# Kernel tuning notes

Measured on AMD Instinct MI355X. Metric: run time of the kernel, lower is better.

## Reference

```python
import jax, jax.numpy as jnp
import numpy as np

N = 250000           # points
B = 2                # batch size
GX, GY, GZ = 256, 256, 32   # voxel grid
SCALES = (2, 4, 6, 8)
CIN = 64             # input_channels
CR = 64              # reduce_channels
CH = CR // 2         # hidden = reduce_channels // 2
COUT = 64            # output_channels


def _cdiv(a, b):
    return -(-a // b)


def setup_inputs() -> dict:
    key = jax.random.key(0)
    ks = jax.random.split(key, 16)
    x = jax.random.normal(ks[0], (N, CIN), jnp.float32)
    bcol = jax.random.randint(ks[1], (N, 1), 0, B)
    xy = jax.random.randint(ks[2], (N, 2), 0, GX)
    z = jax.random.randint(ks[3], (N, 1), 0, GZ)
    coords = jnp.concatenate([bcol, xy, z], axis=1).astype(jnp.int32)
    coords_inv = jnp.arange(N, dtype=jnp.int32)

    def lin(k, fan_in, shape):
        return jax.random.normal(k, shape, jnp.float32) / np.sqrt(fan_in)

    return {
        "x": x,
        "coords": coords,
        "coords_inv": coords_inv,
        "W_red": lin(ks[4], CIN, (CIN, CR)),
        "b_red": jnp.zeros((CR,), jnp.float32),
        "W_pool": lin(ks[5], CR, (len(SCALES), CR, CH)),   # fc_list
        "b_pool": jnp.zeros((len(SCALES), CH), jnp.float32),
        "W_att": lin(ks[6], CH, (len(SCALES), CH, CH)),    # fcs
        "b_att": jnp.zeros((len(SCALES), CH), jnp.float32),
        "W_z": lin(ks[7], CH, (CH, CH)),                   # self.fc (no bias)
        "W_out": lin(ks[8], CH, (CH, CR)),                 # out_fc (no bias)
        "W_l1": lin(ks[9], 2 * CR, (2 * CR, CR)),          # linear_output[0] (no bias)
        "W_l2": lin(ks[10], CR, (CR, COUT)),               # linear_output[2]
        "b_l2": jnp.zeros((COUT,), jnp.float32),
    }


def reference(x, coords, coords_inv, W_red, b_red, W_pool, b_pool,
              W_att, b_att, W_z, W_out, W_l1, W_l2, b_l2):
    # feature_reduce + ReLU
    red = jax.nn.relu(x @ W_red + b_red)              # [N, CR]
    bidx = coords[:, 0].astype(jnp.int32)
    cxyz = coords[:, 1:]

    outs = []
    for j, ps in enumerate(SCALES):
        gx, gy, gz = _cdiv(GX, ps), _cdiv(GY, ps), _cdiv(GZ, ps)
        q = cxyz // ps                                 # quantized coords
        seg = ((bidx * gx + q[:, 0]) * gy + q[:, 1]) * gz + q[:, 2]
        ns = B * gx * gy * gz
        # scatter_mean over voxels at this scale
        sums = jax.ops.segment_sum(red, seg, num_segments=ns)
        cnt = jax.ops.segment_sum(jnp.ones((N, 1), red.dtype), seg, num_segments=ns)
        fkm = sums / jnp.maximum(cnt, 1.0)             # [ns, CR]
        # per-scale MLP then gather back to points
        att = jax.nn.relu(fkm @ W_pool[j] + b_pool[j])[seg]   # [N, CH]
        outs.append(att)

    sf = jnp.stack(outs, axis=1)                       # [N, S, CH]
    feat_Z = jax.nn.relu(sf.sum(axis=1) @ W_z)         # [N, CH]
    att_vecs = jnp.stack([feat_Z @ W_att[j] + b_att[j] for j in range(len(SCALES))], axis=1)
    att_vecs = jax.nn.sigmoid(att_vecs)                # [N, S, CH]
    scale_features = (sf * att_vecs).sum(axis=1) @ W_out   # [N, CR]
    out_f = jnp.concatenate([red, scale_features], axis=1)  # [N, 2*CR]
    proj = jax.nn.relu(out_f @ W_l1) @ W_l2 + b_l2     # [N, COUT]
    return proj[coords_inv]
```

## Files before the change

### kernel.cpp

```cpp
#include <hip/hip_runtime.h>
#include <hip/hip_bf16.h>

#define SEG1 524288
#define SEG2 589824
#define SEG3 612012
#define SEGT 620204

#define K2B0 2048
#define K2B1 2304
#define K2B2 2391
#define K2BT 2423

#define PYRB12 10968

#define SUMS_OFF 32000000ull
#define CNT_OFF  111386112ull
#define ATT_OFF  113866928ull
#define WQ_OFF   153560064ull

typedef __attribute__((ext_vector_type(8))) __bf16 bf16x8;
typedef __attribute__((ext_vector_type(4))) float  f32x4;

__device__ __forceinline__ float bf2f(unsigned short u) {
    union { unsigned int i; float f; } v; v.i = ((unsigned int)u) << 16; return v.f;
}
__device__ __forceinline__ unsigned short f2bf(float f) {
    union { float f; unsigned int i; } v; v.f = f;
    unsigned int r = v.i + 0x7FFF + ((v.i >> 16) & 1);
    return (unsigned short)(r >> 16);
}
__device__ __forceinline__ void atom_pk_bf16(unsigned int* addr, unsigned int pk) {
    asm volatile("global_atomic_pk_add_bf16 %0, %1, off" :: "v"(addr), "v"(pk) : "memory");
}

__device__ __forceinline__ int seg0_of(int b, int cx, int cy, int cz) {
    return ((b*128 + (cx>>1))*128 + (cy>>1))*16 + (cz>>1);
}
__device__ __forceinline__ void seg4(int b, int cx, int cy, int cz, int* s) {
    s[0] =        ((b*128 + (cx>>1))*128 + (cy>>1))*16 + (cz>>1);
    s[1] = SEG1 + ((b*64  + (cx>>2))*64  + (cy>>2))*8  + (cz>>2);
    s[2] = SEG2 + ((b*43  + (cx/6 ))*43  + (cy/6 ))*6  + (cz/6 );
    s[3] = SEG3 + ((b*32  + (cx>>3))*32  + (cy>>3))*4  + (cz>>3);
}

__global__ __launch_bounds__(256) void k0_wprep(
    const float* __restrict__ W_red, const float* __restrict__ W_pool,
    const float* __restrict__ W_z, const float* __restrict__ W_att,
    const float* __restrict__ W_out, const float* __restrict__ W_l1,
    const float* __restrict__ W_l2, char* __restrict__ wq)
{
    int g = blockIdx.x*256 + threadIdx.x;
    if (g < 4096) {
        int idx = g; int k = idx>>6, c = idx&63;
        int byte = (((c<<7)+(k<<1)) ^ ((c&7)<<4));
        *(unsigned short*)(wq + byte) = f2bf(W_red[idx]);
    } else if (g < 12288) {
        int idx = g - 4096; int j = idx>>11, r2 = idx&2047, k = r2>>5, c = r2&31;
        int byte = j*4096 + (((c<<7)+(k<<1)) ^ ((c&7)<<4));
        *(unsigned short*)(wq + 8192 + byte) = f2bf(W_pool[idx]);
    } else if (g < 13312) {
        int idx = g - 12288; int k = idx>>5, c = idx&31;
        *(unsigned short*)(wq + 24576 + ((k>>3)*32+c)*16 + (k&7)*2) = f2bf(W_z[idx]);
    } else if (g < 17408) {
        int idx = g - 13312; int j = idx>>10, rem = idx&1023, k = rem>>5, c = rem&31;
        *(unsigned short*)(wq + 26624 + j*2048 + ((k>>3)*32+c)*16 + (k&7)*2) = f2bf(W_att[idx]);
    } else if (g < 19456) {
        int idx = g - 17408; int k = idx>>6, c = idx&63;
        *(unsigned short*)(wq + 34816 + ((k>>3)*64+c)*16 + (k&7)*2) = f2bf(W_out[idx]);
    } else if (g < 27648) {
        int idx = g - 19456; int k = idx>>6, c = idx&63;
        int byte = (((c<<8)+(k<<1)) ^ ((c&7)<<4));
        *(unsigned short*)(wq + 38912 + byte) = f2bf(W_l1[idx]);
    } else if (g < 31744) {
        int idx = g - 27648; int k = idx>>6, c = idx&63;
        int byte = (((c<<7)+(k<<1)) ^ ((c&7)<<4));
        *(unsigned short*)(wq + 55296 + byte) = f2bf(W_l2[idx]);
    }
}

__global__ __launch_bounds__(256) void k1_mfma(
    const float* __restrict__ x, const int* __restrict__ coords,
    const char* __restrict__ wq, const float* __restrict__ b_red,
    unsigned int* __restrict__ red32, unsigned int* __restrict__ sums_pk,
    float* __restrict__ cnt, int n)
{
    __shared__ uint4 Bw4[512];
    __shared__ uint4 Rt4[512];
    __shared__ int segl[64];
    char* Bw = (char*)Bw4; char* Rt = (char*)Rt4;

    int t = threadIdx.x;
    int i0 = blockIdx.x * 64;

    if (t < 64) {
        int r = i0 + t;
        if (r < n) {
            int4 cv = *(const int4*)&coords[(size_t)r*4];
            int s0 = seg0_of(cv.x, cv.y, cv.z, cv.w);
            segl[t] = s0;
            unsafeAtomicAdd(&cnt[s0], 1.f);
        } else segl[t] = -1;
    }
    {
        const uint4* src = (const uint4*)wq;
        Bw4[t] = src[t];
        Bw4[t + 256] = src[t + 256];
    }
    __syncthreads();

    int lane = t & 63, wv = t >> 6;
    int hi = lane >> 4, lo = lane & 15;
    int arow = wv*16 + lo;
    int grow = i0 + arow;

    bf16x8 afr[2];
    #pragma unroll
    for (int kk = 0; kk < 2; ++kk) {
        unsigned short u[8];
        if (grow < n) {
            const float* xp = x + (size_t)grow*64 + kk*32 + hi*8;
            float4 v0 = *(const float4*)xp;
            float4 v1 = *(const float4*)(xp + 4);
            u[0]=f2bf(v0.x); u[1]=f2bf(v0.y); u[2]=f2bf(v0.z); u[3]=f2bf(v0.w);
            u[4]=f2bf(v1.x); u[5]=f2bf(v1.y); u[6]=f2bf(v1.z); u[7]=f2bf(v1.w);
        } else {
            #pragma unroll
            for (int q = 0; q < 8; ++q) u[q] = 0;
        }
        afr[kk] = *(const bf16x8*)u;
    }

    f32x4 acc[4];
    #pragma unroll
    for (int nt = 0; nt < 4; ++nt) acc[nt] = (f32x4){0.f,0.f,0.f,0.f};
    #pragma unroll
    for (int kk = 0; kk < 2; ++kk) {
        #pragma unroll
        for (int nt = 0; nt < 4; ++nt) {
            int brow = nt*16 + lo;
            int bbyte = ((brow << 7) + ((kk*4 + hi) << 4)) ^ ((brow & 7) << 4);
            bf16x8 bf = *(const bf16x8*)(Bw + bbyte);
            acc[nt] = __builtin_amdgcn_mfma_f32_16x16x32_bf16(afr[kk], bf, acc[nt], 0, 0, 0);
        }
    }
    #pragma unroll
    for (int nt = 0; nt < 4; ++nt) {
        int col = nt*16 + lo;
        float bb = b_red[col];
        #pragma unroll
        for (int r = 0; r < 4; ++r) {
            int row = wv*16 + hi*4 + r;
            int byte = ((row << 7) + (col << 1)) ^ ((row & 7) << 4);
            *(unsigned short*)(Rt + byte) = f2bf(fmaxf(acc[nt][r] + bb, 0.f));
        }
    }
    __syncthreads();

    #pragma unroll
    for (int i2 = 0; i2 < 2; ++i2) {
        int idx = i2*256 + t;
        int row = idx >> 3, ck = idx & 7;
        int r = i0 + row;
        if (r < n) {
            int byte = ((row << 7) + (ck << 4)) ^ ((row & 7) << 4);
            *(uint4*)&red32[(size_t)r*32 + ck*4] = *(const uint4*)(Rt + byte);
        }
    }
    {
        int half = t >> 5, c = t & 31;
        #pragma unroll
        for (int i2 = 0; i2 < 8; ++i2) {
            int p = i2*8 + half;
            int s0_ = segl[p];
            if (s0_ >= 0) {
                int byte = ((p << 7) + (c << 2)) ^ ((p & 7) << 4);
                unsigned int pk = *(const unsigned int*)(Rt + byte);
                atom_pk_bf16(&sums_pk[(size_t)s0_*32 + c], pk);
            }
        }
    }
}

__global__ __launch_bounds__(256) void k_pyramid(
    unsigned int* __restrict__ sums_pk, float* __restrict__ cnt)
{
    int t = threadIdx.x;
    int lane = t & 31;
    int cg = blockIdx.x * 8 + (t >> 5);

    float a0 = 0.f, a1 = 0.f, ca = 0.f;
    int outSeg = -1;

    if (cg < 65536) {
        int r1 = cg;
        int qz = r1 & 7, qy = (r1 >> 3) & 63, qx = (r1 >> 9) & 63, b = r1 >> 15;
        #pragma unroll
        for (int d = 0; d < 8; ++d) {
            int x2 = 2*qx + (d>>2), y2 = 2*qy + ((d>>1)&1), z2 = 2*qz + (d&1);
            int child = ((b*128 + x2)*128 + y2)*16 + z2;
            unsigned int v = sums_pk[(size_t)child*32 + lane];
            a0 += bf2f((unsigned short)(v & 0xffff));
            a1 += bf2f((unsigned short)(v >> 16));
            if (lane == 0) ca += cnt[child];
        }
        outSeg = SEG1 + r1;
    } else {
        int r2 = cg - 65536;
        if (r2 < 22188) {
            int z6 = r2 % 6; int tmp = r2 / 6;
            int y6 = tmp % 43; tmp /= 43;
            int x6 = tmp % 43; int b = tmp / 43;
            for (int dx = 0; dx < 3; ++dx) {
                int x2 = 3*x6 + dx; if (x2 >= 128) break;
                for (int dy = 0; dy < 3; ++dy) {
                    int y2 = 3*y6 + dy; if (y2 >= 128) break;
                    for (int dz = 0; dz < 3; ++dz) {
                        int z2 = 3*z6 + dz; if (z2 >= 16) break;
                        int child = ((b*128 + x2)*128 + y2)*16 + z2;
                        unsigned int v = sums_pk[(size_t)child*32 + lane];
                        a0 += bf2f((unsigned short)(v & 0xffff));
                        a1 += bf2f((unsigned short)(v >> 16));
                        if (lane == 0) ca += cnt[child];
                    }
                }
            }
            outSeg = SEG2 + r2;
        }
    }

    if (outSeg >= 0) {
        unsigned int pk = (unsigned int)f2bf(a0) | ((unsigned int)f2bf(a1) << 16);
        sums_pk[(size_t)outSeg*32 + lane] = pk;
        if (lane == 0) cnt[outSeg] = ca;
    }
}

__global__ __launch_bounds__(256) void k_pyr3(
    unsigned int* __restrict__ sums_pk, float* __restrict__ cnt)
{
    int t = threadIdx.x;
    int lane = t & 31;
    int r3 = blockIdx.x * 8 + (t >> 5);
    int z8 = r3 & 3, y8 = (r3 >> 2) & 31, x8 = (r3 >> 7) & 31, b = r3 >> 12;
    float a0 = 0.f, a1 = 0.f, ca = 0.f;
    #pragma unroll
    for (int d = 0; d < 8; ++d) {
        int qx = 2*x8 + (d>>2), qy = 2*y8 + ((d>>1)&1), qz = 2*z8 + (d&1);
        int child = SEG1 + ((b*64 + qx)*64 + qy)*8 + qz;
        unsigned int v = sums_pk[(size_t)child*32 + lane];
        a0 += bf2f((unsigned short)(v & 0xffff));
        a1 += bf2f((unsigned short)(v >> 16));
        if (lane == 0) ca += cnt[child];
    }
    unsigned int pk = (unsigned int)f2bf(a0) | ((unsigned int)f2bf(a1) << 16);
    sums_pk[(size_t)(SEG3 + r3)*32 + lane] = pk;
    if (lane == 0) cnt[SEG3 + r3] = ca;
}

__global__ __launch_bounds__(256) void k2_mfma(
    const unsigned int* __restrict__ sums_pk, const float* __restrict__ cnt,
    const char* __restrict__ wq, const float* __restrict__ b_pool,
    unsigned short* __restrict__ att)
{
    __shared__ uint4 Bs4[256];
    __shared__ float invs[256];
    char* Bs = (char*)Bs4;

    int t = threadIdx.x;
    int bid = blockIdx.x;
    int j, rel;
    if (bid < K2B0)      { j = 0; rel = bid; }
    else if (bid < K2B1) { j = 1; rel = bid - K2B0; }
    else if (bid < K2B2) { j = 2; rel = bid - K2B1; }
    else                 { j = 3; rel = bid - K2B2; }
    const int segStartT[4] = {0, SEG1, SEG2, SEG3};
    const int segEndT[4]   = {SEG1, SEG2, SEG3, SEGT};
    int s0 = segStartT[j] + rel * 256;
    int sEnd = segEndT[j];

    Bs4[t] = ((const uint4*)(wq + 8192 + j*4096))[t];
    {
        int s = s0 + t;
        invs[t] = (s < sEnd) ? 1.f / fmaxf(cnt[s], 1.f) : 0.f;
    }
    __syncthreads();

    int lane = t & 63, wv = t >> 6;
    int hi = lane >> 4, lo = lane & 15;
    int arow = wv*16 + lo;
    float bp0 = b_pool[j*32 + lo];
    float bp1 = b_pool[j*32 + 16 + lo];

    #pragma unroll
    for (int T = 0; T < 4; ++T) {
        int ts0 = s0 + T*64;
        int srow = ts0 + arow;

        bf16x8 afr[2];
        #pragma unroll
        for (int kk = 0; kk < 2; ++kk) {
            uint4 v = {0u,0u,0u,0u};
            if (srow < sEnd)
                v = *(const uint4*)((const char*)sums_pk + (size_t)srow*128 + kk*64 + hi*16);
            afr[kk] = *(const bf16x8*)&v;
        }

        f32x4 acc[2];
        acc[0] = (f32x4){0.f,0.f,0.f,0.f};
        acc[1] = (f32x4){0.f,0.f,0.f,0.f};
        #pragma unroll
        for (int kk = 0; kk < 2; ++kk) {
            #pragma unroll
            for (int nt = 0; nt < 2; ++nt) {
                int brow = nt*16 + lo;
                int bbyte = ((brow << 7) + ((kk*4 + hi) << 4)) ^ ((brow & 7) << 4);
                bf16x8 bf = *(const bf16x8*)(Bs + bbyte);
                acc[nt] = __builtin_amdgcn_mfma_f32_16x16x32_bf16(afr[kk], bf, acc[nt], 0, 0, 0);
            }
        }
        #pragma unroll
        for (int nt = 0; nt < 2; ++nt) {
            int col = nt*16 + lo;
            float bp = nt ? bp1 : bp0;
            #pragma unroll
            for (int r = 0; r < 4; ++r) {
                int row = T*64 + wv*16 + hi*4 + r;
                int s = s0 + row;
                if (s < sEnd)
                    att[(size_t)s*32 + col] = f2bf(fmaxf(acc[nt][r]*invs[row] + bp, 0.f));
            }
        }
    }
}

__global__ __launch_bounds__(256) void k3a_mfma(
    const int* __restrict__ coords, const unsigned short* __restrict__ att,
    const char* __restrict__ wq, const float* __restrict__ b_att,
    unsigned short* __restrict__ sfeat, int n)
{
    __shared__ uint4 wcomb4[896];
    __shared__ unsigned short sf[8192];
    __shared__ unsigned short AsWs[2048];
    __shared__ unsigned short Fz[2048];
    __shared__ int segl[64][4];
    char* wzp  = (char*)wcomb4;
    char* wattp = (char*)wcomb4 + 2048;
    char* wotp = (char*)wcomb4 + 10240;

    int t = threadIdx.x;
    int i0 = blockIdx.x * 64;
    if (t < 64) {
        int r = i0 + t; if (r >= n) r = n - 1;
        int sg[4]; seg4(coords[r*4], coords[r*4+1], coords[r*4+2], coords[r*4+3], sg);
        segl[t][0]=sg[0]; segl[t][1]=sg[1]; segl[t][2]=sg[2]; segl[t][3]=sg[3];
    }
    {
        const uint4* src = (const uint4*)(wq + 24576);
        for (int idx = t; idx < 896; idx += 256) wcomb4[idx] = src[idx];
    }
    __syncthreads();

    #pragma unroll
    for (int i = 0; i < 4; ++i) {
        int idx = i*256 + t;
        int p = idx >> 4, j = (idx >> 2) & 3, ck = idx & 3;
        int s = segl[p][j];
        uint4 v = *(const uint4*)(att + (size_t)s*32 + ck*8);
        int off = (j*64 + ck*16) ^ (((p>>2)&3) << 4);
        *(uint4*)((char*)sf + p*256 + off) = v;
        unsigned int w_[4] = {v.x, v.y, v.z, v.w};
        float f[8];
        #pragma unroll
        for (int q = 0; q < 4; ++q) {
            f[2*q]   = bf2f((unsigned short)(w_[q] & 0xffff));
            f[2*q+1] = bf2f((unsigned short)(w_[q] >> 16));
        }
        #pragma unroll
        for (int q = 0; q < 8; ++q) {
            f[q] += __shfl_xor(f[q], 4);
            f[q] += __shfl_xor(f[q], 8);
        }
        if (j == 0) {
            unsigned short u8[8];
            #pragma unroll
            for (int q = 0; q < 8; ++q) u8[q] = f2bf(f[q]);
            *(uint4*)((char*)AsWs + (ck*64 + p)*16) = *(const uint4*)u8;
        }
    }
    __syncthreads();

    int lane = t & 63, wv = t >> 6;
    int hi = lane >> 4, lo = lane & 15;
    int arow = wv*16 + lo;

    {
        bf16x8 af = *(const bf16x8*)((char*)AsWs + (hi*64 + arow)*16);
        f32x4 d0 = (f32x4){0.f,0.f,0.f,0.f}, d1 = (f32x4){0.f,0.f,0.f,0.f};
        bf16x8 b0 = *(const bf16x8*)(wzp + (hi*32 + lo)*16);
        bf16x8 b1 = *(const bf16x8*)(wzp + (hi*32 + 16 + lo)*16);
        d0 = __builtin_amdgcn_mfma_f32_16x16x32_bf16(af, b0, d0, 0,0,0);
        d1 = __builtin_amdgcn_mfma_f32_16x16x32_bf16(af, b1, d1, 0,0,0);
        #pragma unroll
        for (int r = 0; r < 4; ++r) {
            int row = wv*16 + hi*4 + r;
            int c0 = lo, c1 = 16 + lo;
            *(unsigned short*)((char*)Fz + ((c0>>3)*64 + row)*16 + (c0&7)*2) = f2bf(fmaxf(d0[r], 0.f));
            *(unsigned short*)((char*)Fz + ((c1>>3)*64 + row)*16 + (c1&7)*2) = f2bf(fmaxf(d1[r], 0.f));
        }
    }
    __syncthreads();
    {
        float wacc[2][4] = {{0.f,0.f,0.f,0.f},{0.f,0.f,0.f,0.f}};
        bf16x8 af = *(const bf16x8*)((char*)Fz + (hi*64 + arow)*16);
        #pragma unroll
        for (int j = 0; j < 4; ++j) {
            f32x4 d0 = (f32x4){0.f,0.f,0.f,0.f}, d1 = (f32x4){0.f,0.f,0.f,0.f};
            bf16x8 b0 = *(const bf16x8*)(wattp + j*2048 + (hi*32 + lo)*16);
            bf16x8 b1 = *(const bf16x8*)(wattp + j*2048 + (hi*32 + 16 + lo)*16);
            d0 = __builtin_amdgcn_mfma_f32_16x16x32_bf16(af, b0, d0, 0,0,0);
            d1 = __builtin_amdgcn_mfma_f32_16x16x32_bf16(af, b1, d1, 0,0,0);
            float ba0 = b_att[j*32 + lo], ba1 = b_att[j*32 + 16 + lo];
            #pragma unroll
            for (int r = 0; r < 4; ++r) {
                int row = wv*16 + hi*4 + r;
                float s0 = 1.f / (1.f + __expf(-(d0[r] + ba0)));
                float s1 = 1.f / (1.f + __expf(-(d1[r] + ba1)));
                float v0 = bf2f(*(const unsigned short*)((char*)sf + row*256 + ((j*64 + lo*2) ^ (hi<<4))));
                float v1 = bf2f(*(const unsigned short*)((char*)sf + row*256 + ((j*64 + (16+lo)*2) ^ (hi<<4))));
                wacc[0][r] += v0 * s0;
                wacc[1][r] += v1 * s1;
            }
        }
        __syncthreads();
        #pragma unroll
        for (int nt = 0; nt < 2; ++nt) {
            int col = nt*16 + lo;
            #pragma unroll
            for (int r = 0; r < 4; ++r) {
                int row = wv*16 + hi*4 + r;
                *(unsigned short*)((char*)AsWs + ((col>>3)*64 + row)*16 + (col&7)*2) = f2bf(wacc[nt][r]);
            }
        }
    }
    __syncthreads();
    {
        bf16x8 af = *(const bf16x8*)((char*)AsWs + (hi*64 + arow)*16);
        #pragma unroll
        for (int nt = 0; nt < 4; ++nt) {
            f32x4 d = (f32x4){0.f,0.f,0.f,0.f};
            bf16x8 bf = *(const bf16x8*)(wotp + (hi*64 + nt*16 + lo)*16);
            d = __builtin_amdgcn_mfma_f32_16x16x32_bf16(af, bf, d, 0,0,0);
            int col = nt*16 + lo;
            #pragma unroll
            for (int r = 0; r < 4; ++r) {
                int row = i0 + wv*16 + hi*4 + r;
                if (row < n) sfeat[(size_t)row*64 + col] = f2bf(d[r]);
            }
        }
    }
}

__global__ __launch_bounds__(256) void k3b_mfma(
    const int* __restrict__ cinv,
    const unsigned short* __restrict__ red, const unsigned short* __restrict__ sfeat,
    const char* __restrict__ wq, const float* __restrict__ b_l2,
    float* __restrict__ out, int n)
{
    __shared__ uint4 wl4[1536];
    __shared__ uint4 hs4[512];
    __shared__ int rl[128];
    char* wl1 = (char*)wl4;
    char* wl2 = (char*)wl4 + 16384;
    char* hs  = (char*)hs4;

    int t = threadIdx.x;
    int i0 = blockIdx.x * 128;
    if (t < 128) { int i = i0 + t; rl[t] = cinv[(i < n) ? i : (n-1)]; }

    {
        const uint4* src = (const uint4*)(wq + 38912);
        for (int idx = t; idx < 1536; idx += 256) wl4[idx] = src[idx];
    }
    __syncthreads();

    int lane = t & 63, wv = t >> 6;
    int hi = lane >> 4, lo = lane & 15;
    int arow = wv*16 + lo;

    #pragma unroll
    for (int T = 0; T < 2; ++T) {
        int grow = rl[T*64 + arow];

        f32x4 acc[4];
        #pragma unroll
        for (int nt = 0; nt < 4; ++nt) acc[nt] = (f32x4){0.f,0.f,0.f,0.f};
        #pragma unroll
        for (int kk = 0; kk < 4; ++kk) {
            int k0 = kk*32 + hi*8;
            const unsigned short* src = (k0 < 64) ? (red + (size_t)grow*64 + k0)
                                                  : (sfeat + (size_t)grow*64 + (k0 - 64));
            bf16x8 af = *(const bf16x8*)src;
            #pragma unroll
            for (int nt = 0; nt < 4; ++nt) {
                int brow = nt*16 + lo;
                int bbyte = ((brow << 8) + ((kk*4 + hi) << 4)) ^ ((brow & 7) << 4);
                bf16x8 bf = *(const bf16x8*)(wl1 + bbyte);
                acc[nt] = __builtin_amdgcn_mfma_f32_16x16x32_bf16(af, bf, acc[nt], 0, 0, 0);
            }
        }
        #pragma unroll
        for (int nt = 0; nt < 4; ++nt) {
            #pragma unroll
            for (int r = 0; r < 4; ++r) {
                int row = wv*16 + hi*4 + r;
                int col = nt*16 + lo;
                int byte = ((row << 7) + (col << 1)) ^ ((row & 7) << 4);
                *(unsigned short*)(hs + byte) = f2bf(fmaxf(acc[nt][r], 0.f));
            }
        }
        __syncthreads();

        f32x4 acc2[4];
        #pragma unroll
        for (int nt = 0; nt < 4; ++nt) acc2[nt] = (f32x4){0.f,0.f,0.f,0.f};
        #pragma unroll
        for (int kk = 0; kk < 2; ++kk) {
            int abyte = ((arow << 7) + ((kk*4 + hi) << 4)) ^ ((arow & 7) << 4);
            bf16x8 af = *(const bf16x8*)(hs + abyte);
            #pragma unroll
            for (int nt = 0; nt < 4; ++nt) {
                int brow = nt*16 + lo;
                int bbyte = ((brow << 7) + ((kk*4 + hi) << 4)) ^ ((brow & 7) << 4);
                bf16x8 bf = *(const bf16x8*)(wl2 + bbyte);
                acc2[nt] = __builtin_amdgcn_mfma_f32_16x16x32_bf16(af, bf, acc2[nt], 0, 0, 0);
            }
        }
        #pragma unroll
        for (int nt = 0; nt < 4; ++nt) {
            int col = nt*16 + lo;
            float bl = b_l2[col];
            #pragma unroll
            for (int r = 0; r < 4; ++r) {
                int row = i0 + T*64 + wv*16 + hi*4 + r;
                if (row < n) out[(size_t)row*64 + col] = acc2[nt][r] + bl;
            }
        }
        __syncthreads();
    }
}

extern "C" void kernel_launch(void* const* d_in, const int* in_sizes, int n_in,
                              void* d_out, int out_size, void* d_ws, size_t ws_size,
                              hipStream_t stream) {
    const float* x      = (const float*)d_in[0];
    const int*   coords = (const int*)  d_in[1];
    const int*   cinv   = (const int*)  d_in[2];
    const float* W_red  = (const float*)d_in[3];
    const float* b_red  = (const float*)d_in[4];
    const float* W_pool = (const float*)d_in[5];
    const float* b_pool = (const float*)d_in[6];
    const float* W_att  = (const float*)d_in[7];
    const float* b_att  = (const float*)d_in[8];
    const float* W_z    = (const float*)d_in[9];
    const float* W_out  = (const float*)d_in[10];
    const float* W_l1   = (const float*)d_in[11];
    const float* W_l2   = (const float*)d_in[12];
    const float* b_l2   = (const float*)d_in[13];
    float* out = (float*)d_out;
    int n = in_sizes[0] / 64;

    char* wsb = (char*)d_ws;
    unsigned int*   red32   = (unsigned int*)(wsb);
    unsigned short* red     = (unsigned short*)(wsb);
    unsigned int*   sums_pk = (unsigned int*)(wsb + SUMS_OFF);
    float*          cnt     = (float*)(wsb + CNT_OFF);
    unsigned short* att     = (unsigned short*)(wsb + ATT_OFF);
    char*           wq      = wsb + WQ_OFF;
    unsigned short* sfeat   = (unsigned short*)(wsb + SUMS_OFF);

    k0_wprep<<<124, 256, 0, stream>>>(W_red, W_pool, W_z, W_att, W_out, W_l1, W_l2, wq);
    hipMemsetAsync(sums_pk, 0, (size_t)SEG1 * 128ull, stream);
    hipMemsetAsync(cnt, 0, (size_t)SEG1 * 4ull, stream);

    k1_mfma<<<(n + 63) / 64, 256, 0, stream>>>(x, coords, wq, b_red, red32, sums_pk, cnt, n);
    k_pyramid<<<PYRB12, 256, 0, stream>>>(sums_pk, cnt);
    k_pyr3<<<1024, 256, 0, stream>>>(sums_pk, cnt);
    k2_mfma<<<K2BT, 256, 0, stream>>>(sums_pk, cnt, wq, b_pool, att);
    k3a_mfma<<<(n + 63) / 64, 256, 0, stream>>>(coords, att, wq, b_att, sfeat, n);
    k3b_mfma<<<(n + 127) / 128, 256, 0, stream>>>(cinv, red, sfeat, wq, b_l2, out, n);
}
```

Baseline: 207.8 us.

## Compact non-empty finest voxels for per-scale MLP and tile pyramid reduction

Adds a compaction kernel that uses a wave ballot and an atomic counter to build a list of non-empty finest-scale voxels. The scale-0 MLP kernel then works only on listed segments, and blocks past the count exit early. It also merges the scale-2 and scale-3 pyramid reductions into spatially tiled blocks (3x3x3 coarse cells plus 2x2x2 cells at scale 6) to improve locality on the child reads. This costs an extra kernel launch and memset, gather-indexed reads, and non-deterministic list ordering.

```diff
diff --git a/kernel.cpp b/kernel.cpp
--- a/kernel.cpp
+++ b/kernel.cpp
@@ -11,12 +11,14 @@
 #define K2B2 2391
 #define K2BT 2423
 
-#define PYRB12 10968
+#define PYRF_B 2904
 
 #define SUMS_OFF 32000000ull
 #define CNT_OFF  111386112ull
 #define ATT_OFF  113866928ull
 #define WQ_OFF   153560064ull
+#define CTR_OFF  153623552ull
+#define LIST_OFF 153623808ull
 
 typedef __attribute__((ext_vector_type(8))) __bf16 bf16x8;
 typedef __attribute__((ext_vector_type(4))) float  f32x4;
@@ -181,57 +183,79 @@
     }
 }
 
-__global__ __launch_bounds__(256) void k_pyramid(
+__global__ __launch_bounds__(256) void kc_compact(
+    const float* __restrict__ cnt, int* __restrict__ list, int* __restrict__ counter)
+{
+    int s = blockIdx.x*256 + threadIdx.x;
+    bool ne = (s < SEG1) && (cnt[s] > 0.f);
+    unsigned long long mask = __ballot(ne);
+    int lane = threadIdx.x & 63;
+    int nw = __popcll(mask);
+    int base = 0;
+    if (lane == 0 && nw) base = atomicAdd(counter, nw);
+    base = __shfl(base, 0);
+    if (ne) {
+        int pos = base + __popcll(mask & ((1ull << lane) - 1ull));
+        list[pos] = s;
+    }
+}
+
+__global__ __launch_bounds__(256) void k_pyr12(
     unsigned int* __restrict__ sums_pk, float* __restrict__ cnt)
 {
     int t = threadIdx.x;
-    int lane = t & 31;
-    int cg = blockIdx.x * 8 + (t >> 5);
-
-    float a0 = 0.f, a1 = 0.f, ca = 0.f;
-    int outSeg = -1;
-
-    if (cg < 65536) {
-        int r1 = cg;
-        int qz = r1 & 7, qy = (r1 >> 3) & 63, qx = (r1 >> 9) & 63, b = r1 >> 15;
-        #pragma unroll
-        for (int d = 0; d < 8; ++d) {
-            int x2 = 2*qx + (d>>2), y2 = 2*qy + ((d>>1)&1), z2 = 2*qz + (d&1);
-            int child = ((b*128 + x2)*128 + y2)*16 + z2;
-            unsigned int v = sums_pk[(size_t)child*32 + lane];
-            a0 += bf2f((unsigned short)(v & 0xffff));
-            a1 += bf2f((unsigned short)(v >> 16));
-            if (lane == 0) ca += cnt[child];
-        }
-        outSeg = SEG1 + r1;
-    } else {
-        int r2 = cg - 65536;
-        if (r2 < 22188) {
-            int z6 = r2 % 6; int tmp = r2 / 6;
-            int y6 = tmp % 43; tmp /= 43;
-            int x6 = tmp % 43; int b = tmp / 43;
-            for (int dx = 0; dx < 3; ++dx) {
-                int x2 = 3*x6 + dx; if (x2 >= 128) break;
-                for (int dy = 0; dy < 3; ++dy) {
-                    int y2 = 3*y6 + dy; if (y2 >= 128) break;
-                    for (int dz = 0; dz < 3; ++dz) {
-                        int z2 = 3*z6 + dz; if (z2 >= 16) break;
-                        int child = ((b*128 + x2)*128 + y2)*16 + z2;
-                        unsigned int v = sums_pk[(size_t)child*32 + lane];
-                        a0 += bf2f((unsigned short)(v & 0xffff));
-                        a1 += bf2f((unsigned short)(v >> 16));
-                        if (lane == 0) ca += cnt[child];
+    int c = t & 31;
+    int h = t >> 5;
+    int chunk = blockIdx.x;
+    int oz = chunk % 3; int tmp = chunk / 3;
+    int oy = tmp % 22; tmp /= 22;
+    int ox = tmp % 22; int b = tmp / 22;
+
+    for (int cc = h; cc < 35; cc += 8) {
+        float a0 = 0.f, a1 = 0.f, ca = 0.f;
+        int outSeg = -1;
+        if (cc < 27) {
+            int lz = cc % 3, ly = (cc/3) % 3, lx = cc/9;
+            int qx = ox*3 + lx, qy = oy*3 + ly, qz = oz*3 + lz;
+            if (qx < 64 && qy < 64 && qz < 8) {
+                #pragma unroll
+                for (int d = 0; d < 8; ++d) {
+                    int x2 = 2*qx + (d>>2), y2 = 2*qy + ((d>>1)&1), z2 = 2*qz + (d&1);
+                    int child = ((b*128 + x2)*128 + y2)*16 + z2;
+                    unsigned int v = sums_pk[(size_t)child*32 + c];
+                    a0 += bf2f((unsigned short)(v & 0xffff));
+                    a1 += bf2f((unsigned short)(v >> 16));
+                    if (c == 0) ca += cnt[child];
+                }
+                outSeg = SEG1 + ((b*64 + qx)*64 + qy)*8 + qz;
+            }
+        } else {
+            int m = cc - 27;
+            int mz = m & 1, my = (m>>1)&1, mx = m>>2;
+            int x6 = ox*2 + mx, y6 = oy*2 + my, z6 = oz*2 + mz;
+            if (x6 < 43 && y6 < 43 && z6 < 6) {
+                for (int dx = 0; dx < 3; ++dx) {
+                    int x2 = 3*x6 + dx; if (x2 >= 128) break;
+                    for (int dy = 0; dy < 3; ++dy) {
+                        int y2 = 3*y6 + dy; if (y2 >= 128) break;
+                        for (int dz = 0; dz < 3; ++dz) {
+                            int z2 = 3*z6 + dz; if (z2 >= 16) break;
+                            int child = ((b*128 + x2)*128 + y2)*16 + z2;
+                            unsigned int v = sums_pk[(size_t)child*32 + c];
+                            a0 += bf2f((unsigned short)(v & 0xffff));
+                            a1 += bf2f((unsigned short)(v >> 16));
+                            if (c == 0) ca += cnt[child];
+                        }
                     }
                 }
-            }
-            outSeg = SEG2 + r2;
-        }
-    }
-
-    if (outSeg >= 0) {
-        unsigned int pk = (unsigned int)f2bf(a0) | ((unsigned int)f2bf(a1) << 16);
-        sums_pk[(size_t)outSeg*32 + lane] = pk;
-        if (lane == 0) cnt[outSeg] = ca;
+                outSeg = SEG2 + ((b*43 + x6)*43 + y6)*6 + z6;
+            }
+        }
+        if (outSeg >= 0) {
+            unsigned int pk = (unsigned int)f2bf(a0) | ((unsigned int)f2bf(a1) << 16);
+            sums_pk[(size_t)outSeg*32 + c] = pk;
+            if (c == 0) cnt[outSeg] = ca;
+        }
     }
 }
 
@@ -260,10 +284,12 @@
 __global__ __launch_bounds__(256) void k2_mfma(
     const unsigned int* __restrict__ sums_pk, const float* __restrict__ cnt,
     const char* __restrict__ wq, const float* __restrict__ b_pool,
+    const int* __restrict__ list, const int* __restrict__ counter,
     unsigned short* __restrict__ att)
 {
     __shared__ uint4 Bs4[256];
     __shared__ float invs[256];
+    __shared__ int   segL[256];
     char* Bs = (char*)Bs4;
 
     int t = threadIdx.x;
@@ -273,15 +299,24 @@
     else if (bid < K2B1) { j = 1; rel = bid - K2B0; }
     else if (bid < K2B2) { j = 2; rel = bid - K2B1; }
     else                 { j = 3; rel = bid - K2B2; }
-    const int segStartT[4] = {0, SEG1, SEG2, SEG3};
-    const int segEndT[4]   = {SEG1, SEG2, SEG3, SEGT};
-    int s0 = segStartT[j] + rel * 256;
-    int sEnd = segEndT[j];
+
+    if (j == 0 && rel*256 >= counter[0]) return;
 
     Bs4[t] = ((const uint4*)(wq + 8192 + j*4096))[t];
     {
-        int s = s0 + t;
-        invs[t] = (s < sEnd) ? 1.f / fmaxf(cnt[s], 1.f) : 0.f;
+        int seg;
+        if (j == 0) {
+            int count = counter[0];
+            int pos = rel*256 + t;
+            seg = (pos < count) ? list[pos] : -1;
+        } else {
+            const int segStartT[4] = {0, SEG1, SEG2, SEG3};
+            const int segEndT[4]   = {SEG1, SEG2, SEG3, SEGT};
+            int s = segStartT[j] + rel*256 + t;
+            seg = (s < segEndT[j]) ? s : -1;
+        }
+        segL[t] = seg;
+        invs[t] = (seg >= 0) ? 1.f / fmaxf(cnt[seg], 1.f) : 0.f;
     }
     __syncthreads();
 
@@ -293,14 +328,13 @@
 
     #pragma unroll
     for (int T = 0; T < 4; ++T) {
-        int ts0 = s0 + T*64;
-        int srow = ts0 + arow;
+        int srow = segL[T*64 + arow];
 
         bf16x8 afr[2];
         #pragma unroll
         for (int kk = 0; kk < 2; ++kk) {
             uint4 v = {0u,0u,0u,0u};
-            if (srow < sEnd)
+            if (srow >= 0)
                 v = *(const uint4*)((const char*)sums_pk + (size_t)srow*128 + kk*64 + hi*16);
             afr[kk] = *(const bf16x8*)&v;
         }
@@ -325,8 +359,8 @@
             #pragma unroll
             for (int r = 0; r < 4; ++r) {
                 int row = T*64 + wv*16 + hi*4 + r;
-                int s = s0 + row;
-                if (s < sEnd)
+                int s = segL[row];
+                if (s >= 0)
                     att[(size_t)s*32 + col] = f2bf(fmaxf(acc[nt][r]*invs[row] + bp, 0.f));
             }
         }
@@ -576,16 +610,20 @@
     float*          cnt     = (float*)(wsb + CNT_OFF);
     unsigned short* att     = (unsigned short*)(wsb + ATT_OFF);
     char*           wq      = wsb + WQ_OFF;
+    int*            counter = (int*)(wsb + CTR_OFF);
+    int*            list    = (int*)(wsb + LIST_OFF);
     unsigned short* sfeat   = (unsigned short*)(wsb + SUMS_OFF);
 
     k0_wprep<<<124, 256, 0, stream>>>(W_red, W_pool, W_z, W_att, W_out, W_l1, W_l2, wq);
     hipMemsetAsync(sums_pk, 0, (size_t)SEG1 * 128ull, stream);
     hipMemsetAsync(cnt, 0, (size_t)SEG1 * 4ull, stream);
+    hipMemsetAsync(counter, 0, 4, stream);
 
     k1_mfma<<<(n + 63) / 64, 256, 0, stream>>>(x, coords, wq, b_red, red32, sums_pk, cnt, n);
-    k_pyramid<<<PYRB12, 256, 0, stream>>>(sums_pk, cnt);
+    kc_compact<<<2048, 256, 0, stream>>>(cnt, list, counter);
+    k_pyr12<<<PYRF_B, 256, 0, stream>>>(sums_pk, cnt);
     k_pyr3<<<1024, 256, 0, stream>>>(sums_pk, cnt);
-    k2_mfma<<<K2BT, 256, 0, stream>>>(sums_pk, cnt, wq, b_pool, att);
+    k2_mfma<<<K2BT, 256, 0, stream>>>(sums_pk, cnt, wq, b_pool, list, counter, att);
     k3a_mfma<<<(n + 63) / 64, 256, 0, stream>>>(coords, att, wq, b_att, sfeat, n);
     k3b_mfma<<<(n + 127) / 128, 256, 0, stream>>>(cinv, red, sfeat, wq, b_l2, out, n);
 }
```

New measurement: 316.1 us. 52.1% more time.

## Tile pyramid build so scale-4 and scale-6 cells share 12x12x12 fine-voxel chunks

Applied to the files above, without the earlier changes.

The scale-4 and scale-6 pooling pyramid is restructured so each block owns a 12x12x12 region of scale-2 voxels. It computes all 27 scale-4 parents and 8 scale-6 parents inside that region, so both levels read the same child rows close together in time and can hit in cache. The cost is fewer blocks (2904 instead of 10968), a per-warp loop with some idle warps (35 tasks over 8 warps), and extra bounds checks for partial tiles at the grid edges.

```diff
diff --git a/kernel.cpp b/kernel.cpp
--- a/kernel.cpp
+++ b/kernel.cpp
@@ -11,7 +11,7 @@
 #define K2B2 2391
 #define K2BT 2423
 
-#define PYRB12 10968
+#define PYRF_B 2904
 
 #define SUMS_OFF 32000000ull
 #define CNT_OFF  111386112ull
@@ -181,57 +181,62 @@
     }
 }
 
-__global__ __launch_bounds__(256) void k_pyramid(
+__global__ __launch_bounds__(256) void k_pyr12(
     unsigned int* __restrict__ sums_pk, float* __restrict__ cnt)
 {
     int t = threadIdx.x;
-    int lane = t & 31;
-    int cg = blockIdx.x * 8 + (t >> 5);
-
-    float a0 = 0.f, a1 = 0.f, ca = 0.f;
-    int outSeg = -1;
-
-    if (cg < 65536) {
-        int r1 = cg;
-        int qz = r1 & 7, qy = (r1 >> 3) & 63, qx = (r1 >> 9) & 63, b = r1 >> 15;
-        #pragma unroll
-        for (int d = 0; d < 8; ++d) {
-            int x2 = 2*qx + (d>>2), y2 = 2*qy + ((d>>1)&1), z2 = 2*qz + (d&1);
-            int child = ((b*128 + x2)*128 + y2)*16 + z2;
-            unsigned int v = sums_pk[(size_t)child*32 + lane];
-            a0 += bf2f((unsigned short)(v & 0xffff));
-            a1 += bf2f((unsigned short)(v >> 16));
-            if (lane == 0) ca += cnt[child];
-        }
-        outSeg = SEG1 + r1;
-    } else {
-        int r2 = cg - 65536;
-        if (r2 < 22188) {
-            int z6 = r2 % 6; int tmp = r2 / 6;
-            int y6 = tmp % 43; tmp /= 43;
-            int x6 = tmp % 43; int b = tmp / 43;
-            for (int dx = 0; dx < 3; ++dx) {
-                int x2 = 3*x6 + dx; if (x2 >= 128) break;
-                for (int dy = 0; dy < 3; ++dy) {
-                    int y2 = 3*y6 + dy; if (y2 >= 128) break;
-                    for (int dz = 0; dz < 3; ++dz) {
-                        int z2 = 3*z6 + dz; if (z2 >= 16) break;
-                        int child = ((b*128 + x2)*128 + y2)*16 + z2;
-                        unsigned int v = sums_pk[(size_t)child*32 + lane];
-                        a0 += bf2f((unsigned short)(v & 0xffff));
-                        a1 += bf2f((unsigned short)(v >> 16));
-                        if (lane == 0) ca += cnt[child];
+    int c = t & 31;
+    int h = t >> 5;
+    int chunk = blockIdx.x;
+    int oz = chunk % 3; int tmp = chunk / 3;
+    int oy = tmp % 22; tmp /= 22;
+    int ox = tmp % 22; int b = tmp / 22;
+
+    for (int cc = h; cc < 35; cc += 8) {
+        float a0 = 0.f, a1 = 0.f, ca = 0.f;
+        int outSeg = -1;
+        if (cc < 27) {
+            int lz = cc % 3, ly = (cc/3) % 3, lx = cc/9;
+            int qx = ox*3 + lx, qy = oy*3 + ly, qz = oz*3 + lz;
+            if (qx < 64 && qy < 64 && qz < 8) {
+                #pragma unroll
+                for (int d = 0; d < 8; ++d) {
+                    int x2 = 2*qx + (d>>2), y2 = 2*qy + ((d>>1)&1), z2 = 2*qz + (d&1);
+                    int child = ((b*128 + x2)*128 + y2)*16 + z2;
+                    unsigned int v = sums_pk[(size_t)child*32 + c];
+                    a0 += bf2f((unsigned short)(v & 0xffff));
+                    a1 += bf2f((unsigned short)(v >> 16));
+                    if (c == 0) ca += cnt[child];
+                }
+                outSeg = SEG1 + ((b*64 + qx)*64 + qy)*8 + qz;
+            }
+        } else {
+            int m = cc - 27;
+            int mz = m & 1, my = (m>>1)&1, mx = m>>2;
+            int x6 = ox*2 + mx, y6 = oy*2 + my, z6 = oz*2 + mz;
+            if (x6 < 43 && y6 < 43 && z6 < 6) {
+                for (int dx = 0; dx < 3; ++dx) {
+                    int x2 = 3*x6 + dx; if (x2 >= 128) break;
+                    for (int dy = 0; dy < 3; ++dy) {
+                        int y2 = 3*y6 + dy; if (y2 >= 128) break;
+                        for (int dz = 0; dz < 3; ++dz) {
+                            int z2 = 3*z6 + dz; if (z2 >= 16) break;
+                            int child = ((b*128 + x2)*128 + y2)*16 + z2;
+                            unsigned int v = sums_pk[(size_t)child*32 + c];
+                            a0 += bf2f((unsigned short)(v & 0xffff));
+                            a1 += bf2f((unsigned short)(v >> 16));
+                            if (c == 0) ca += cnt[child];
+                        }
                     }
                 }
-            }
-            outSeg = SEG2 + r2;
-        }
-    }
-
-    if (outSeg >= 0) {
-        unsigned int pk = (unsigned int)f2bf(a0) | ((unsigned int)f2bf(a1) << 16);
-        sums_pk[(size_t)outSeg*32 + lane] = pk;
-        if (lane == 0) cnt[outSeg] = ca;
+                outSeg = SEG2 + ((b*43 + x6)*43 + y6)*6 + z6;
+            }
+        }
+        if (outSeg >= 0) {
+            unsigned int pk = (unsigned int)f2bf(a0) | ((unsigned int)f2bf(a1) << 16);
+            sums_pk[(size_t)outSeg*32 + c] = pk;
+            if (c == 0) cnt[outSeg] = ca;
+        }
     }
 }
 
@@ -583,7 +588,7 @@
     hipMemsetAsync(cnt, 0, (size_t)SEG1 * 4ull, stream);
 
     k1_mfma<<<(n + 63) / 64, 256, 0, stream>>>(x, coords, wq, b_red, red32, sums_pk, cnt, n);
-    k_pyramid<<<PYRB12, 256, 0, stream>>>(sums_pk, cnt);
+    k_pyr12<<<PYRF_B, 256, 0, stream>>>(sums_pk, cnt);
     k_pyr3<<<1024, 256, 0, stream>>>(sums_pk, cnt);
     k2_mfma<<<K2BT, 256, 0, stream>>>(sums_pk, cnt, wq, b_pool, att);
     k3a_mfma<<<(n + 63) / 64, 256, 0, stream>>>(coords, att, wq, b_att, sfeat, n);
```

Result: slower. 222.3 us (+7.0%).
